# Kernel optimization log

Measured on AMD Instinct MI355X. Metric: run time of the kernel, lower is better.

Reference implementation:

```python
import jax, jax.numpy as jnp
import numpy as np

N_NODES = 100000


def gcn_layer(x, W, b, src, dst, norm, n):
    # x: [N, Fin] -> linear transform then normalized scatter-add aggregation
    h = x @ W                                   # [N, Fout]
    msgs = h[src] * norm[:, None]               # [E+N, Fout] edge messages
    out = jax.ops.segment_sum(msgs, dst, num_segments=n)
    return out + b


def _build_graph(edge_index, n):
    # add self loops (PyG GCNConv default)
    loops = jnp.arange(n, dtype=edge_index.dtype)
    src = jnp.concatenate([edge_index[0], loops])
    dst = jnp.concatenate([edge_index[1], loops])
    deg = jax.ops.segment_sum(jnp.ones_like(dst, dtype=jnp.float32), dst, num_segments=n)
    dis = jnp.where(deg > 0, jax.lax.rsqrt(deg), 0.0)  # deg^{-1/2}
    norm = dis[src] * dis[dst]                  # symmetric normalization per edge
    return src, dst, norm


def setup_inputs() -> dict:
    key = jax.random.key(0)
    ks = jax.random.split(key, 8)
    x = jax.random.normal(ks[0], (N_NODES, 3), dtype=jnp.float32)
    edge_index = jax.random.randint(ks[1], (2, 6400000), 0, N_NODES, dtype=jnp.int32)
    def glorot(k, fin, fout):
        s = jnp.sqrt(6.0 / (fin + fout))
        return jax.random.uniform(k, (fin, fout), jnp.float32, -s, s)
    return {
        "x": x,
        "edge_index": edge_index,
        "W1": glorot(ks[2], 3, 32), "b1": jnp.zeros((32,), jnp.float32),
        "W2": glorot(ks[3], 32, 32), "b2": jnp.zeros((32,), jnp.float32),
        "W3": glorot(ks[4], 32, 1), "b3": jnp.zeros((1,), jnp.float32),
    }


def reference(x, edge_index, W1, b1, W2, b2, W3, b3):
    n = x.shape[0]
    src, dst, norm = _build_graph(edge_index, n)
    h = jax.nn.relu(gcn_layer(x, W1, b1, src, dst, norm, n))
    h = jax.nn.relu(gcn_layer(h, W2, b2, src, dst, norm, n))
    return gcn_layer(h, W3, b3, src, dst, norm, n)
```

## Files before the change

### kernel.cpp

```cpp
#include <hip/hip_runtime.h>
#include <hip/hip_fp16.h>


#define BLK 256
#define SB 1280
#define CHUNK 5000
#define BKT 128
#define NBKT 782
#define MAXNB 1024
#define BUFSZ 15360

__global__ void k_hist(const int* __restrict__ dst, int* __restrict__ hist, int E) {
    __shared__ int lh[NBKT];
    for (int b = threadIdx.x; b < NBKT; b += blockDim.x) lh[b] = 0;
    __syncthreads();
    int beg = blockIdx.x * CHUNK;
    int end = min(E, beg + CHUNK);
    int nq = (end - beg) >> 2;
    const int4* d4 = (const int4*)(dst + beg);
    for (int i = threadIdx.x; i < nq; i += blockDim.x) {
        int4 d = d4[i];
        atomicAdd(&lh[d.x >> 7], 1);
        atomicAdd(&lh[d.y >> 7], 1);
        atomicAdd(&lh[d.z >> 7], 1);
        atomicAdd(&lh[d.w >> 7], 1);
    }
    for (int e = beg + (nq << 2) + threadIdx.x; e < end; e += blockDim.x)
        atomicAdd(&lh[dst[e] >> 7], 1);
    __syncthreads();
    for (int b = threadIdx.x; b < NBKT; b += blockDim.x)
        hist[(size_t)blockIdx.x * NBKT + b] = lh[b];
}

__global__ void k_scanA(int* __restrict__ hist, int* __restrict__ btot, int NB) {
    int b = blockIdx.x, t = threadIdx.x;
    int base = t * 5;
    int v0 = hist[(size_t)(base + 0) * NB + b];
    int v1 = hist[(size_t)(base + 1) * NB + b];
    int v2 = hist[(size_t)(base + 2) * NB + b];
    int v3 = hist[(size_t)(base + 3) * NB + b];
    int v4 = hist[(size_t)(base + 4) * NB + b];
    int s = v0 + v1 + v2 + v3 + v4;
    int lane = t & 63, w = t >> 6;
    int x = s;
#pragma unroll
    for (int off = 1; off < 64; off <<= 1) {
        int u = __shfl_up(x, off, 64);
        if (lane >= off) x += u;
    }
    __shared__ int wsum[4];
    if (lane == 63) wsum[w] = x;
    __syncthreads();
    int woff = 0;
    for (int k = 0; k < 4; k++) woff += (k < w) ? wsum[k] : 0;
    int run = woff + x - s;
    hist[(size_t)(base + 0) * NB + b] = run;  run += v0;
    hist[(size_t)(base + 1) * NB + b] = run;  run += v1;
    hist[(size_t)(base + 2) * NB + b] = run;  run += v2;
    hist[(size_t)(base + 3) * NB + b] = run;  run += v3;
    hist[(size_t)(base + 4) * NB + b] = run;  run += v4;
    if (t == 255) btot[b] = run;
}

__global__ void k_scanB(const int* __restrict__ btot, int* __restrict__ bbase,
                        int NB, int E) {
    __shared__ int sh[MAXNB];
    int t = threadIdx.x;
    int v = (t < NB) ? btot[t] : 0;
    sh[t] = v;
    __syncthreads();
    for (int off = 1; off < MAXNB; off <<= 1) {
        int u = (t >= off) ? sh[t - off] : 0;
        __syncthreads();
        sh[t] += u;
        __syncthreads();
    }
    if (t < NB) bbase[t] = sh[t] - v;
    if (t == 0) bbase[NB] = E;
}

__global__ void k_bsort(const int* __restrict__ src, const int* __restrict__ dst,
                        const int* __restrict__ hist, const int* __restrict__ bbase,
                        unsigned int* __restrict__ packed, int E) {
    __shared__ unsigned int bufB[CHUNK];
    __shared__ unsigned short binarr2[CHUNK];
    __shared__ int cnt[NBKT];
    __shared__ int off[NBKT];
    __shared__ int cur[NBKT];
    __shared__ int gbase[NBKT];
    __shared__ int wsum[4];
    int t = threadIdx.x;
    int beg = blockIdx.x * CHUNK;
    int end = min(E, beg + CHUNK);
    int len = end - beg;
    for (int b = t; b < NBKT; b += blockDim.x) {
        cnt[b] = 0;
        gbase[b] = bbase[b] + hist[(size_t)blockIdx.x * NBKT + b];
    }
    __syncthreads();
    {
        int nq = len >> 2;
        const int4* d4 = (const int4*)(dst + beg);
        for (int i = t; i < nq; i += blockDim.x) {
            int4 d = d4[i];
            atomicAdd(&cnt[d.x >> 7], 1);
            atomicAdd(&cnt[d.y >> 7], 1);
            atomicAdd(&cnt[d.z >> 7], 1);
            atomicAdd(&cnt[d.w >> 7], 1);
        }
        for (int i = (nq << 2) + t; i < len; i += blockDim.x)
            atomicAdd(&cnt[dst[beg + i] >> 7], 1);
    }
    __syncthreads();
    {
        int base = t * 4;
        int v0 = (base + 0 < NBKT) ? cnt[base + 0] : 0;
        int v1 = (base + 1 < NBKT) ? cnt[base + 1] : 0;
        int v2 = (base + 2 < NBKT) ? cnt[base + 2] : 0;
        int v3 = (base + 3 < NBKT) ? cnt[base + 3] : 0;
        int s = v0 + v1 + v2 + v3;
        int lane = t & 63, w = t >> 6;
        int x = s;
#pragma unroll
        for (int o = 1; o < 64; o <<= 1) {
            int u = __shfl_up(x, o, 64);
            if (lane >= o) x += u;
        }
        if (lane == 63) wsum[w] = x;
        __syncthreads();
        int woff = 0;
        for (int k = 0; k < 4; k++) woff += (k < w) ? wsum[k] : 0;
        int run = woff + x - s;
        if (base + 0 < NBKT) { off[base + 0] = run; cur[base + 0] = run; } run += v0;
        if (base + 1 < NBKT) { off[base + 1] = run; cur[base + 1] = run; } run += v1;
        if (base + 2 < NBKT) { off[base + 2] = run; cur[base + 2] = run; } run += v2;
        if (base + 3 < NBKT) { off[base + 3] = run; cur[base + 3] = run; } run += v3;
    }
    __syncthreads();
    for (int i = t; i < len; i += blockDim.x) {
        int d = dst[beg + i];
        int s = src[beg + i];
        int b = d >> 7;
        int pos = atomicAdd(&cur[b], 1);
        bufB[pos] = (unsigned)s | ((unsigned)(d & 127) << 17);
        binarr2[pos] = (unsigned short)b;
    }
    __syncthreads();
    for (int i = t; i < len; i += blockDim.x) {
        int b = binarr2[i];
        packed[gbase[b] + i - off[b]] = bufB[i];
    }
}

__global__ void k_sort(unsigned int* __restrict__ packed, const int* __restrict__ bbase,
                       const float* __restrict__ x, float* __restrict__ dis,
                       float4* __restrict__ y4, int* __restrict__ rowptr, int N, int E) {
    __shared__ unsigned int buf[BUFSZ];
    __shared__ int cnt[4 * BKT];
    __shared__ int cur[4 * BKT];
    __shared__ int wsum[4];
    int b = blockIdx.x, t = threadIdx.x;
    int beg = bbase[b], end = bbase[b + 1];
    int len = end - beg;
    for (int i = t; i < len; i += blockDim.x) buf[i] = packed[beg + i];
    cnt[t] = 0; cnt[t + 256] = 0;
    __syncthreads();
    for (int i = t; i < len; i += blockDim.x) {
        unsigned v = buf[i];
        int key = (int)((v >> 17) << 2) | (int)((v & 0x1FFFFu) >> 15);
        atomicAdd(&cnt[key], 1);
    }
    __syncthreads();
    {
        int v0 = cnt[2 * t], v1 = cnt[2 * t + 1];
        int s = v0 + v1;
        int lane = t & 63, w = t >> 6;
        int xs = s;
#pragma unroll
        for (int o = 1; o < 64; o <<= 1) {
            int u = __shfl_up(xs, o, 64);
            if (lane >= o) xs += u;
        }
        if (lane == 63) wsum[w] = xs;
        __syncthreads();
        int woff = 0;
        for (int k = 0; k < 4; k++) woff += (k < w) ? wsum[k] : 0;
        int run = woff + xs - s;
        cur[2 * t] = run;
        cur[2 * t + 1] = run + v0;
    }
    __syncthreads();
    if (t < BKT) {
        int excl = cur[4 * t];
        int v = cnt[4 * t] + cnt[4 * t + 1] + cnt[4 * t + 2] + cnt[4 * t + 3];
        int gi = b * BKT + t;
        if (gi < N) {
            rowptr[gi] = beg + excl;
            float di = rsqrtf((float)v + 1.0f);
            dis[gi] = di;
            float4 y;
            y.x = di * x[3 * gi + 0];
            y.y = di * x[3 * gi + 1];
            y.z = di * x[3 * gi + 2];
            y.w = 0.0f;
            y4[gi] = y;
        }
    }
    __syncthreads();
    for (int i = t; i < len; i += blockDim.x) {
        unsigned vv = buf[i];
        int key = (int)((vv >> 17) << 2) | (int)((vv & 0x1FFFFu) >> 15);
        int pos = atomicAdd(&cur[key], 1);
        packed[beg + pos] = vv & 0x1FFFF;
    }
    if (b == 0 && t == 0) rowptr[N] = E;
}

__global__ void k_l1(const unsigned int* __restrict__ csr, const int* __restrict__ rowptr,
                     const float4* __restrict__ y4, const float* __restrict__ dis,
                     const float* __restrict__ W1, const float* __restrict__ b1,
                     __half* __restrict__ g, int N) {
    int t = blockIdx.x * blockDim.x + threadIdx.x;
    int i = t >> 5, j = t & 31;
    if (i >= N) return;
    int beg = rowptr[i], end = rowptr[i + 1];
    float ax = 0.f, ay = 0.f, az = 0.f;
    for (int e = beg + j; e < end; e += 32) {
        float4 yv = y4[csr[e]];
        ax += yv.x; ay += yv.y; az += yv.z;
    }
#pragma unroll
    for (int m = 16; m >= 1; m >>= 1) {
        ax += __shfl_xor(ax, m, 32);
        ay += __shfl_xor(ay, m, 32);
        az += __shfl_xor(az, m, 32);
    }
    float di = dis[i];
    float4 ys = y4[i];
    float a0 = di * (ax + ys.x);
    float a1 = di * (ay + ys.y);
    float a2 = di * (az + ys.z);
    float h = b1[j] + a0 * W1[j] + a1 * W1[32 + j] + a2 * W1[64 + j];
    g[(size_t)i * 32 + j] = __float2half(di * fmaxf(h, 0.f));
}

__device__ __forceinline__ void acc4(float& c0, float& c1, float& c2, float& c3,
                                     uint2 r) {
    __half2 a = *(const __half2*)&r.x;
    __half2 b = *(const __half2*)&r.y;
    float2 fa = __half22float2(a);
    float2 fb = __half22float2(b);
    c0 += fa.x; c1 += fa.y; c2 += fb.x; c3 += fb.y;
}

__global__ void k_l2(const unsigned int* __restrict__ csr, const int* __restrict__ rowptr,
                     const __half* __restrict__ g, const float* __restrict__ dis,
                     const float* __restrict__ W2, const float* __restrict__ b2,
                     const float* __restrict__ W3, float* __restrict__ q, int N) {
    int t = blockIdx.x * blockDim.x + threadIdx.x;
    int i = t >> 3, j = t & 7;
    if (i >= N) return;
    int beg = rowptr[i], end = rowptr[i + 1];
    const uint2* g2 = (const uint2*)g;
    float c0 = 0.f, c1 = 0.f, c2 = 0.f, c3 = 0.f;
    int e = beg;
    for (; e + 8 <= end; e += 8) {
        int s0 = (int)csr[e + 0], s1 = (int)csr[e + 1];
        int s2 = (int)csr[e + 2], s3 = (int)csr[e + 3];
        int s4 = (int)csr[e + 4], s5 = (int)csr[e + 5];
        int s6 = (int)csr[e + 6], s7 = (int)csr[e + 7];
        uint2 r0 = g2[s0 * 8 + j];
        uint2 r1 = g2[s1 * 8 + j];
        uint2 r2 = g2[s2 * 8 + j];
        uint2 r3 = g2[s3 * 8 + j];
        uint2 r4 = g2[s4 * 8 + j];
        uint2 r5 = g2[s5 * 8 + j];
        uint2 r6 = g2[s6 * 8 + j];
        uint2 r7 = g2[s7 * 8 + j];
        acc4(c0, c1, c2, c3, r0);
        acc4(c0, c1, c2, c3, r1);
        acc4(c0, c1, c2, c3, r2);
        acc4(c0, c1, c2, c3, r3);
        acc4(c0, c1, c2, c3, r4);
        acc4(c0, c1, c2, c3, r5);
        acc4(c0, c1, c2, c3, r6);
        acc4(c0, c1, c2, c3, r7);
    }
    for (; e < end; e++) {
        int s = (int)csr[e];
        uint2 r = g2[s * 8 + j];
        acc4(c0, c1, c2, c3, r);
    }
    float di = dis[i];
    uint2 rs = g2[i * 8 + j];
    float2 sa = __half22float2(*(const __half2*)&rs.x);
    float2 sb = __half22float2(*(const __half2*)&rs.y);
    float a0 = di * (c0 + sa.x);
    float a1 = di * (c1 + sa.y);
    float a2 = di * (c2 + sb.x);
    float a3 = di * (c3 + sb.y);
    int m = 4 * j;
    float o0 = b2[m + 0], o1 = b2[m + 1], o2 = b2[m + 2], o3 = b2[m + 3];
#pragma unroll
    for (int kl = 0; kl < 8; kl++) {
        float x0 = __shfl(a0, kl, 8);
        float x1 = __shfl(a1, kl, 8);
        float x2 = __shfl(a2, kl, 8);
        float x3 = __shfl(a3, kl, 8);
        const float* w0 = W2 + (4 * kl) * 32 + m;
        o0 = fmaf(x0, w0[0], fmaf(x1, w0[32], fmaf(x2, w0[64], fmaf(x3, w0[96], o0))));
        o1 = fmaf(x0, w0[1], fmaf(x1, w0[33], fmaf(x2, w0[65], fmaf(x3, w0[97], o1))));
        o2 = fmaf(x0, w0[2], fmaf(x1, w0[34], fmaf(x2, w0[66], fmaf(x3, w0[98], o2))));
        o3 = fmaf(x0, w0[3], fmaf(x1, w0[35], fmaf(x2, w0[67], fmaf(x3, w0[99], o3))));
    }
    float cc = fmaxf(o0, 0.f) * W3[m + 0] + fmaxf(o1, 0.f) * W3[m + 1]
             + fmaxf(o2, 0.f) * W3[m + 2] + fmaxf(o3, 0.f) * W3[m + 3];
    cc += __shfl_xor(cc, 1, 8);
    cc += __shfl_xor(cc, 2, 8);
    cc += __shfl_xor(cc, 4, 8);
    if (j == 0) q[i] = di * cc;
}

__global__ void k_l3(const unsigned int* __restrict__ csr, const int* __restrict__ rowptr,
                     const float* __restrict__ q, const float* __restrict__ dis,
                     const float* __restrict__ b3, float* __restrict__ out, int N) {
    int t = blockIdx.x * blockDim.x + threadIdx.x;
    int i = t >> 5, j = t & 31;
    if (i >= N) return;
    int beg = rowptr[i], end = rowptr[i + 1];
    float acc = 0.f;
    for (int e = beg + j; e < end; e += 32)
        acc += q[csr[e]];
#pragma unroll
    for (int m = 16; m >= 1; m >>= 1)
        acc += __shfl_xor(acc, m, 32);
    if (j == 0) out[i] = dis[i] * (acc + q[i]) + b3[0];
}

extern "C" void kernel_launch(void* const* d_in, const int* in_sizes, int n_in,
                              void* d_out, int out_size, void* d_ws, size_t ws_size,
                              hipStream_t stream) {
    const float* x  = (const float*)d_in[0];
    const int*   ei = (const int*)d_in[1];
    const float* W1 = (const float*)d_in[2];
    const float* b1 = (const float*)d_in[3];
    const float* W2 = (const float*)d_in[4];
    const float* b2 = (const float*)d_in[5];
    const float* W3 = (const float*)d_in[6];
    const float* b3 = (const float*)d_in[7];
    float* out = (float*)d_out;

    int N = in_sizes[0] / 3;
    int E = in_sizes[1] / 2;
    const int* src = ei;
    const int* dst = ei + E;

    char* w = (char*)d_ws;
#define CARVE(nbytes) w; w += (((size_t)(nbytes) + 255) & ~(size_t)255)
    int*   hist   = (int*)  CARVE((size_t)SB * NBKT * 4);
    int*   btot   = (int*)  CARVE((size_t)MAXNB * 4);
    int*   bbase  = (int*)  CARVE((size_t)(MAXNB + 1) * 4);
    int*   rowptr = (int*)  CARVE((size_t)(N + 1) * 4);
    float* dis    = (float*)CARVE((size_t)N * 4);
    float* y4     = (float*)CARVE((size_t)N * 16);
    __half* g     = (__half*)CARVE((size_t)N * 32 * 2);
    float* q      = (float*)CARVE((size_t)N * 4);
    unsigned int* packed = (unsigned int*)CARVE((size_t)E * 4);
#undef CARVE

    k_hist <<<SB, BLK, 0, stream>>>(dst, hist, E);
    k_scanA<<<NBKT, BLK, 0, stream>>>(hist, btot, NBKT);
    k_scanB<<<1, MAXNB, 0, stream>>>(btot, bbase, NBKT, E);
    k_bsort<<<SB, BLK, 0, stream>>>(src, dst, hist, bbase, packed, E);
    k_sort <<<NBKT, BLK, 0, stream>>>(packed, bbase, x, dis, (float4*)y4, rowptr, N, E);

    long long tn = (long long)N * 32;
    unsigned gn = (unsigned)((tn + BLK - 1) / BLK);
    long long tn8 = (long long)N * 8;
    unsigned gn8 = (unsigned)((tn8 + BLK - 1) / BLK);
    k_l1<<<gn,  BLK, 0, stream>>>(packed, rowptr, (const float4*)y4, dis, W1, b1, g, N);
    k_l2<<<gn8, BLK, 0, stream>>>(packed, rowptr, g, dis, W2, b2, W3, q, N);
    k_l3<<<gn,  BLK, 0, stream>>>(packed, rowptr, q, dis, b3, out, N);
}
```

Before: 348.8 us.

## Split layer-2 gather into two source-halves passes and reuse histogram counts

Within each destination row, edges are now sorted so sources below 50000 come first, and a per-node midpoint is recorded. Layer-2 aggregation then runs as two kernels: the first gathers only from the lower half of the feature table and writes partial sums, the second gathers from the upper half, adds the partials and applies the dense layers. Each pass touches half of the fp16 feature table, which should improve L2/cache hit rates for the random gathers. The cost is an extra 12.8MB partial write and read, plus a second launch. The bucket-sort kernel also derives per-block bucket counts from adjacent histogram prefix values instead of recounting destinations with shared atomics.

```diff
diff --git a/kernel.cpp b/kernel.cpp
--- a/kernel.cpp
+++ b/kernel.cpp
@@ -9,6 +9,9 @@
 #define NBKT 782
 #define MAXNB 1024
 #define BUFSZ 15360
+#define HALF 50000
+
+typedef float fvec4 __attribute__((ext_vector_type(4)));
 
 __global__ void k_hist(const int* __restrict__ dst, int* __restrict__ hist, int E) {
     __shared__ int lh[NBKT];
@@ -80,7 +83,8 @@
 }
 
 __global__ void k_bsort(const int* __restrict__ src, const int* __restrict__ dst,
-                        const int* __restrict__ hist, const int* __restrict__ bbase,
+                        const int* __restrict__ hist, const int* __restrict__ btot,
+                        const int* __restrict__ bbase,
                         unsigned int* __restrict__ packed, int E) {
     __shared__ unsigned int bufB[CHUNK];
     __shared__ unsigned short binarr2[CHUNK];
@@ -93,23 +97,12 @@
     int beg = blockIdx.x * CHUNK;
     int end = min(E, beg + CHUNK);
     int len = end - beg;
+    int last = (blockIdx.x + 1 == gridDim.x);
     for (int b = t; b < NBKT; b += blockDim.x) {
-        cnt[b] = 0;
-        gbase[b] = bbase[b] + hist[(size_t)blockIdx.x * NBKT + b];
-    }
-    __syncthreads();
-    {
-        int nq = len >> 2;
-        const int4* d4 = (const int4*)(dst + beg);
-        for (int i = t; i < nq; i += blockDim.x) {
-            int4 d = d4[i];
-            atomicAdd(&cnt[d.x >> 7], 1);
-            atomicAdd(&cnt[d.y >> 7], 1);
-            atomicAdd(&cnt[d.z >> 7], 1);
-            atomicAdd(&cnt[d.w >> 7], 1);
-        }
-        for (int i = (nq << 2) + t; i < len; i += blockDim.x)
-            atomicAdd(&cnt[dst[beg + i] >> 7], 1);
+        int my = hist[(size_t)blockIdx.x * NBKT + b];
+        int nx = last ? btot[b] : hist[(size_t)(blockIdx.x + 1) * NBKT + b];
+        cnt[b] = nx - my;
+        gbase[b] = bbase[b] + my;
     }
     __syncthreads();
     {
@@ -154,28 +147,29 @@
 
 __global__ void k_sort(unsigned int* __restrict__ packed, const int* __restrict__ bbase,
                        const float* __restrict__ x, float* __restrict__ dis,
-                       float4* __restrict__ y4, int* __restrict__ rowptr, int N, int E) {
+                       float4* __restrict__ y4, int* __restrict__ rowptr,
+                       int* __restrict__ qmid, int N, int E) {
     __shared__ unsigned int buf[BUFSZ];
-    __shared__ int cnt[4 * BKT];
-    __shared__ int cur[4 * BKT];
+    __shared__ int cnt[2 * BKT];
+    __shared__ int cur[2 * BKT];
     __shared__ int wsum[4];
     int b = blockIdx.x, t = threadIdx.x;
     int beg = bbase[b], end = bbase[b + 1];
     int len = end - beg;
     for (int i = t; i < len; i += blockDim.x) buf[i] = packed[beg + i];
-    cnt[t] = 0; cnt[t + 256] = 0;
+    cnt[t] = 0;
     __syncthreads();
     for (int i = t; i < len; i += blockDim.x) {
         unsigned v = buf[i];
-        int key = (int)((v >> 17) << 2) | (int)((v & 0x1FFFFu) >> 15);
+        int s = (int)(v & 0x1FFFFu);
+        int key = (int)((v >> 17) << 1) | (s >= HALF);
         atomicAdd(&cnt[key], 1);
     }
     __syncthreads();
     {
-        int v0 = cnt[2 * t], v1 = cnt[2 * t + 1];
-        int s = v0 + v1;
+        int v0 = cnt[t];
         int lane = t & 63, w = t >> 6;
-        int xs = s;
+        int xs = v0;
 #pragma unroll
         for (int o = 1; o < 64; o <<= 1) {
             int u = __shfl_up(xs, o, 64);
@@ -185,17 +179,16 @@
         __syncthreads();
         int woff = 0;
         for (int k = 0; k < 4; k++) woff += (k < w) ? wsum[k] : 0;
-        int run = woff + xs - s;
-        cur[2 * t] = run;
-        cur[2 * t + 1] = run + v0;
+        cur[t] = woff + xs - v0;
     }
     __syncthreads();
     if (t < BKT) {
-        int excl = cur[4 * t];
-        int v = cnt[4 * t] + cnt[4 * t + 1] + cnt[4 * t + 2] + cnt[4 * t + 3];
+        int excl = cur[2 * t];
+        int v = cnt[2 * t] + cnt[2 * t + 1];
         int gi = b * BKT + t;
         if (gi < N) {
             rowptr[gi] = beg + excl;
+            qmid[gi]   = beg + cur[2 * t + 1];
             float di = rsqrtf((float)v + 1.0f);
             dis[gi] = di;
             float4 y;
@@ -209,9 +202,10 @@
     __syncthreads();
     for (int i = t; i < len; i += blockDim.x) {
         unsigned vv = buf[i];
-        int key = (int)((vv >> 17) << 2) | (int)((vv & 0x1FFFFu) >> 15);
+        int s = (int)(vv & 0x1FFFFu);
+        int key = (int)((vv >> 17) << 1) | (s >= HALF);
         int pos = atomicAdd(&cur[key], 1);
-        packed[beg + pos] = vv & 0x1FFFF;
+        packed[beg + pos] = (unsigned)s;
     }
     if (b == 0 && t == 0) rowptr[N] = E;
 }
@@ -253,16 +247,10 @@
     c0 += fa.x; c1 += fa.y; c2 += fb.x; c3 += fb.y;
 }
 
-__global__ void k_l2(const unsigned int* __restrict__ csr, const int* __restrict__ rowptr,
-                     const __half* __restrict__ g, const float* __restrict__ dis,
-                     const float* __restrict__ W2, const float* __restrict__ b2,
-                     const float* __restrict__ W3, float* __restrict__ q, int N) {
-    int t = blockIdx.x * blockDim.x + threadIdx.x;
-    int i = t >> 3, j = t & 7;
-    if (i >= N) return;
-    int beg = rowptr[i], end = rowptr[i + 1];
-    const uint2* g2 = (const uint2*)g;
-    float c0 = 0.f, c1 = 0.f, c2 = 0.f, c3 = 0.f;
+__device__ __forceinline__ void gath(const unsigned int* __restrict__ csr,
+                                     const uint2* __restrict__ g2, int j,
+                                     int beg, int end,
+                                     float& c0, float& c1, float& c2, float& c3) {
     int e = beg;
     for (; e + 8 <= end; e += 8) {
         int s0 = (int)csr[e + 0], s1 = (int)csr[e + 1];
@@ -291,6 +279,73 @@
         uint2 r = g2[s * 8 + j];
         acc4(c0, c1, c2, c3, r);
     }
+}
+
+__global__ void k_l2a(const unsigned int* __restrict__ csr, const int* __restrict__ rowptr,
+                      const int* __restrict__ qmid, const __half* __restrict__ g,
+                      fvec4* __restrict__ part4, int N) {
+    int t = blockIdx.x * blockDim.x + threadIdx.x;
+    int i = t >> 3, j = t & 7;
+    if (i >= N) return;
+    float c0 = 0.f, c1 = 0.f, c2 = 0.f, c3 = 0.f;
+    gath(csr, (const uint2*)g, j, rowptr[i], qmid[i], c0, c1, c2, c3);
+    fvec4 p = {c0, c1, c2, c3};
+    __builtin_nontemporal_store(p, &part4[(size_t)i * 8 + j]);
+}
+
+__global__ void k_l2b(const unsigned int* __restrict__ csr, const int* __restrict__ rowptr,
+                      const int* __restrict__ qmid, const __half* __restrict__ g,
+                      const float* __restrict__ dis, const fvec4* __restrict__ part4,
+                      const float* __restrict__ W2, const float* __restrict__ b2,
+                      const float* __restrict__ W3, float* __restrict__ q, int N) {
+    int t = blockIdx.x * blockDim.x + threadIdx.x;
+    int i = t >> 3, j = t & 7;
+    if (i >= N) return;
+    const uint2* g2 = (const uint2*)g;
+    float c0 = 0.f, c1 = 0.f, c2 = 0.f, c3 = 0.f;
+    gath(csr, g2, j, qmid[i], rowptr[i + 1], c0, c1, c2, c3);
+    fvec4 p = __builtin_nontemporal_load(&part4[(size_t)i * 8 + j]);
+    c0 += p.x; c1 += p.y; c2 += p.z; c3 += p.w;
+    float di = dis[i];
+    uint2 rs = g2[i * 8 + j];
+    float2 sa = __half22float2(*(const __half2*)&rs.x);
+    float2 sb = __half22float2(*(const __half2*)&rs.y);
+    float a0 = di * (c0 + sa.x);
+    float a1 = di * (c1 + sa.y);
+    float a2 = di * (c2 + sb.x);
+    float a3 = di * (c3 + sb.y);
+    int m = 4 * j;
+    float o0 = b2[m + 0], o1 = b2[m + 1], o2 = b2[m + 2], o3 = b2[m + 3];
+#pragma unroll
+    for (int kl = 0; kl < 8; kl++) {
+        float x0 = __shfl(a0, kl, 8);
+        float x1 = __shfl(a1, kl, 8);
+        float x2 = __shfl(a2, kl, 8);
+        float x3 = __shfl(a3, kl, 8);
+        const float* w0 = W2 + (4 * kl) * 32 + m;
+        o0 = fmaf(x0, w0[0], fmaf(x1, w0[32], fmaf(x2, w0[64], fmaf(x3, w0[96], o0))));
+        o1 = fmaf(x0, w0[1], fmaf(x1, w0[33], fmaf(x2, w0[65], fmaf(x3, w0[97], o1))));
+        o2 = fmaf(x0, w0[2], fmaf(x1, w0[34], fmaf(x2, w0[66], fmaf(x3, w0[98], o2))));
+        o3 = fmaf(x0, w0[3], fmaf(x1, w0[35], fmaf(x2, w0[67], fmaf(x3, w0[99], o3))));
+    }
+    float cc = fmaxf(o0, 0.f) * W3[m + 0] + fmaxf(o1, 0.f) * W3[m + 1]
+             + fmaxf(o2, 0.f) * W3[m + 2] + fmaxf(o3, 0.f) * W3[m + 3];
+    cc += __shfl_xor(cc, 1, 8);
+    cc += __shfl_xor(cc, 2, 8);
+    cc += __shfl_xor(cc, 4, 8);
+    if (j == 0) q[i] = di * cc;
+}
+
+__global__ void k_l2f(const unsigned int* __restrict__ csr, const int* __restrict__ rowptr,
+                      const __half* __restrict__ g, const float* __restrict__ dis,
+                      const float* __restrict__ W2, const float* __restrict__ b2,
+                      const float* __restrict__ W3, float* __restrict__ q, int N) {
+    int t = blockIdx.x * blockDim.x + threadIdx.x;
+    int i = t >> 3, j = t & 7;
+    if (i >= N) return;
+    const uint2* g2 = (const uint2*)g;
+    float c0 = 0.f, c1 = 0.f, c2 = 0.f, c3 = 0.f;
+    gath(csr, g2, j, rowptr[i], rowptr[i + 1], c0, c1, c2, c3);
     float di = dis[i];
     uint2 rs = g2[i * 8 + j];
     float2 sa = __half22float2(*(const __half2*)&rs.x);
@@ -366,19 +421,31 @@
     __half* g     = (__half*)CARVE((size_t)N * 32 * 2);
     float* q      = (float*)CARVE((size_t)N * 4);
     unsigned int* packed = (unsigned int*)CARVE((size_t)E * 4);
+    int*   qmid   = (int*)  CARVE((size_t)N * 4);
+    fvec4* part4  = (fvec4*)CARVE((size_t)N * 32 * 4);
+    size_t need_split = (size_t)(w - (char*)d_ws);
 #undef CARVE
+    int use_split = (ws_size >= need_split);
+    if (!use_split) qmid = hist;
 
     k_hist <<<SB, BLK, 0, stream>>>(dst, hist, E);
     k_scanA<<<NBKT, BLK, 0, stream>>>(hist, btot, NBKT);
     k_scanB<<<1, MAXNB, 0, stream>>>(btot, bbase, NBKT, E);
-    k_bsort<<<SB, BLK, 0, stream>>>(src, dst, hist, bbase, packed, E);
-    k_sort <<<NBKT, BLK, 0, stream>>>(packed, bbase, x, dis, (float4*)y4, rowptr, N, E);
+    k_bsort<<<SB, BLK, 0, stream>>>(src, dst, hist, btot, bbase, packed, E);
+    k_sort <<<NBKT, BLK, 0, stream>>>(packed, bbase, x, dis, (float4*)y4, rowptr,
+                                      qmid, N, E);
 
     long long tn = (long long)N * 32;
     unsigned gn = (unsigned)((tn + BLK - 1) / BLK);
     long long tn8 = (long long)N * 8;
     unsigned gn8 = (unsigned)((tn8 + BLK - 1) / BLK);
-    k_l1<<<gn,  BLK, 0, stream>>>(packed, rowptr, (const float4*)y4, dis, W1, b1, g, N);
-    k_l2<<<gn8, BLK, 0, stream>>>(packed, rowptr, g, dis, W2, b2, W3, q, N);
-    k_l3<<<gn,  BLK, 0, stream>>>(packed, rowptr, q, dis, b3, out, N);
-}
+    k_l1<<<gn, BLK, 0, stream>>>(packed, rowptr, (const float4*)y4, dis, W1, b1, g, N);
+    if (use_split) {
+        k_l2a<<<gn8, BLK, 0, stream>>>(packed, rowptr, qmid, g, part4, N);
+        k_l2b<<<gn8, BLK, 0, stream>>>(packed, rowptr, qmid, g, dis, part4,
+                                       W2, b2, W3, q, N);
+    } else {
+        k_l2f<<<gn8, BLK, 0, stream>>>(packed, rowptr, g, dis, W2, b2, W3, q, N);
+    }
+    k_l3<<<gn, BLK, 0, stream>>>(packed, rowptr, q, dis, b3, out, N);
+}
```

After: 356.1 us. 2.1% more time.

## Reuse scanned histogram in bucket sort, simplify fine sort, split accumulators

Applied to the files above, without the earlier changes.

k_bsort now derives its per-chunk bucket counts from the exclusive-scanned histogram, taking the next chunk's row or btot for the last block, so it no longer re-reads dst and recounts with shared atomics. k_sort replaces the two-level 512-key sort with a single 128-key counting sort, fuses the global load into the count pass, and shrinks the shared buffer. Both kernels launch with 512 threads. k_l2 spreads its gather accumulation over four independent accumulator sets to shorten the dependent add chains. Risks: the smaller BUFSZ may overflow for heavy buckets, and k_sort now orders each row's edges only by destination rather than also by a coarse source key, which may hurt gather locality in the aggregation layers.

```diff
diff --git a/kernel.cpp b/kernel.cpp
--- a/kernel.cpp
+++ b/kernel.cpp
@@ -3,12 +3,13 @@
 
 
 #define BLK 256
+#define BLK2 512
 #define SB 1280
 #define CHUNK 5000
 #define BKT 128
 #define NBKT 782
 #define MAXNB 1024
-#define BUFSZ 15360
+#define BUFSZ 10240
 
 __global__ void k_hist(const int* __restrict__ dst, int* __restrict__ hist, int E) {
     __shared__ int lh[NBKT];
@@ -80,7 +81,8 @@
 }
 
 __global__ void k_bsort(const int* __restrict__ src, const int* __restrict__ dst,
-                        const int* __restrict__ hist, const int* __restrict__ bbase,
+                        const int* __restrict__ hist, const int* __restrict__ btot,
+                        const int* __restrict__ bbase,
                         unsigned int* __restrict__ packed, int E) {
     __shared__ unsigned int bufB[CHUNK];
     __shared__ unsigned short binarr2[CHUNK];
@@ -88,37 +90,24 @@
     __shared__ int off[NBKT];
     __shared__ int cur[NBKT];
     __shared__ int gbase[NBKT];
-    __shared__ int wsum[4];
+    __shared__ int wsum[8];
     int t = threadIdx.x;
     int beg = blockIdx.x * CHUNK;
     int end = min(E, beg + CHUNK);
     int len = end - beg;
+    int last = (blockIdx.x + 1 == gridDim.x);
     for (int b = t; b < NBKT; b += blockDim.x) {
-        cnt[b] = 0;
-        gbase[b] = bbase[b] + hist[(size_t)blockIdx.x * NBKT + b];
+        int my = hist[(size_t)blockIdx.x * NBKT + b];
+        int nx = last ? btot[b] : hist[(size_t)(blockIdx.x + 1) * NBKT + b];
+        cnt[b] = nx - my;
+        gbase[b] = bbase[b] + my;
     }
     __syncthreads();
     {
-        int nq = len >> 2;
-        const int4* d4 = (const int4*)(dst + beg);
-        for (int i = t; i < nq; i += blockDim.x) {
-            int4 d = d4[i];
-            atomicAdd(&cnt[d.x >> 7], 1);
-            atomicAdd(&cnt[d.y >> 7], 1);
-            atomicAdd(&cnt[d.z >> 7], 1);
-            atomicAdd(&cnt[d.w >> 7], 1);
-        }
-        for (int i = (nq << 2) + t; i < len; i += blockDim.x)
-            atomicAdd(&cnt[dst[beg + i] >> 7], 1);
-    }
-    __syncthreads();
-    {
-        int base = t * 4;
+        int base = t * 2;
         int v0 = (base + 0 < NBKT) ? cnt[base + 0] : 0;
         int v1 = (base + 1 < NBKT) ? cnt[base + 1] : 0;
-        int v2 = (base + 2 < NBKT) ? cnt[base + 2] : 0;
-        int v3 = (base + 3 < NBKT) ? cnt[base + 3] : 0;
-        int s = v0 + v1 + v2 + v3;
+        int s = v0 + v1;
         int lane = t & 63, w = t >> 6;
         int x = s;
 #pragma unroll
@@ -129,12 +118,10 @@
         if (lane == 63) wsum[w] = x;
         __syncthreads();
         int woff = 0;
-        for (int k = 0; k < 4; k++) woff += (k < w) ? wsum[k] : 0;
+        for (int k = 0; k < 8; k++) woff += (k < w) ? wsum[k] : 0;
         int run = woff + x - s;
         if (base + 0 < NBKT) { off[base + 0] = run; cur[base + 0] = run; } run += v0;
         if (base + 1 < NBKT) { off[base + 1] = run; cur[base + 1] = run; } run += v1;
-        if (base + 2 < NBKT) { off[base + 2] = run; cur[base + 2] = run; } run += v2;
-        if (base + 3 < NBKT) { off[base + 3] = run; cur[base + 3] = run; } run += v3;
     }
     __syncthreads();
     for (int i = t; i < len; i += blockDim.x) {
@@ -156,47 +143,40 @@
                        const float* __restrict__ x, float* __restrict__ dis,
                        float4* __restrict__ y4, int* __restrict__ rowptr, int N, int E) {
     __shared__ unsigned int buf[BUFSZ];
-    __shared__ int cnt[4 * BKT];
-    __shared__ int cur[4 * BKT];
-    __shared__ int wsum[4];
+    __shared__ int cnt[BKT];
+    __shared__ int cur[BKT];
+    __shared__ int wsum[2];
     int b = blockIdx.x, t = threadIdx.x;
     int beg = bbase[b], end = bbase[b + 1];
     int len = end - beg;
-    for (int i = t; i < len; i += blockDim.x) buf[i] = packed[beg + i];
-    cnt[t] = 0; cnt[t + 256] = 0;
+    if (t < BKT) cnt[t] = 0;
     __syncthreads();
     for (int i = t; i < len; i += blockDim.x) {
-        unsigned v = buf[i];
-        int key = (int)((v >> 17) << 2) | (int)((v & 0x1FFFFu) >> 15);
-        atomicAdd(&cnt[key], 1);
-    }
-    __syncthreads();
-    {
-        int v0 = cnt[2 * t], v1 = cnt[2 * t + 1];
-        int s = v0 + v1;
-        int lane = t & 63, w = t >> 6;
-        int xs = s;
+        unsigned v = packed[beg + i];
+        buf[i] = v;
+        atomicAdd(&cnt[v >> 17], 1);
+    }
+    __syncthreads();
+    int v0 = 0, xs = 0;
+    if (t < BKT) {
+        v0 = cnt[t];
+        xs = v0;
 #pragma unroll
         for (int o = 1; o < 64; o <<= 1) {
             int u = __shfl_up(xs, o, 64);
-            if (lane >= o) xs += u;
+            if ((t & 63) >= o) xs += u;
         }
-        if (lane == 63) wsum[w] = xs;
-        __syncthreads();
-        int woff = 0;
-        for (int k = 0; k < 4; k++) woff += (k < w) ? wsum[k] : 0;
-        int run = woff + xs - s;
-        cur[2 * t] = run;
-        cur[2 * t + 1] = run + v0;
+        if ((t & 63) == 63) wsum[t >> 6] = xs;
     }
     __syncthreads();
     if (t < BKT) {
-        int excl = cur[4 * t];
-        int v = cnt[4 * t] + cnt[4 * t + 1] + cnt[4 * t + 2] + cnt[4 * t + 3];
+        int woff = (t >= 64) ? wsum[0] : 0;
+        int excl = woff + xs - v0;
+        cur[t] = excl;
         int gi = b * BKT + t;
         if (gi < N) {
             rowptr[gi] = beg + excl;
-            float di = rsqrtf((float)v + 1.0f);
+            float di = rsqrtf((float)v0 + 1.0f);
             dis[gi] = di;
             float4 y;
             y.x = di * x[3 * gi + 0];
@@ -209,8 +189,7 @@
     __syncthreads();
     for (int i = t; i < len; i += blockDim.x) {
         unsigned vv = buf[i];
-        int key = (int)((vv >> 17) << 2) | (int)((vv & 0x1FFFFu) >> 15);
-        int pos = atomicAdd(&cur[key], 1);
+        int pos = atomicAdd(&cur[vv >> 17], 1);
         packed[beg + pos] = vv & 0x1FFFF;
     }
     if (b == 0 && t == 0) rowptr[N] = E;
@@ -262,7 +241,10 @@
     if (i >= N) return;
     int beg = rowptr[i], end = rowptr[i + 1];
     const uint2* g2 = (const uint2*)g;
-    float c0 = 0.f, c1 = 0.f, c2 = 0.f, c3 = 0.f;
+    float pa0 = 0.f, pa1 = 0.f, pa2 = 0.f, pa3 = 0.f;
+    float pb0 = 0.f, pb1 = 0.f, pb2 = 0.f, pb3 = 0.f;
+    float pc0 = 0.f, pc1 = 0.f, pc2 = 0.f, pc3 = 0.f;
+    float pd0 = 0.f, pd1 = 0.f, pd2 = 0.f, pd3 = 0.f;
     int e = beg;
     for (; e + 8 <= end; e += 8) {
         int s0 = (int)csr[e + 0], s1 = (int)csr[e + 1];
@@ -277,20 +259,24 @@
         uint2 r5 = g2[s5 * 8 + j];
         uint2 r6 = g2[s6 * 8 + j];
         uint2 r7 = g2[s7 * 8 + j];
-        acc4(c0, c1, c2, c3, r0);
-        acc4(c0, c1, c2, c3, r1);
-        acc4(c0, c1, c2, c3, r2);
-        acc4(c0, c1, c2, c3, r3);
-        acc4(c0, c1, c2, c3, r4);
-        acc4(c0, c1, c2, c3, r5);
-        acc4(c0, c1, c2, c3, r6);
-        acc4(c0, c1, c2, c3, r7);
+        acc4(pa0, pa1, pa2, pa3, r0);
+        acc4(pb0, pb1, pb2, pb3, r1);
+        acc4(pc0, pc1, pc2, pc3, r2);
+        acc4(pd0, pd1, pd2, pd3, r3);
+        acc4(pa0, pa1, pa2, pa3, r4);
+        acc4(pb0, pb1, pb2, pb3, r5);
+        acc4(pc0, pc1, pc2, pc3, r6);
+        acc4(pd0, pd1, pd2, pd3, r7);
     }
     for (; e < end; e++) {
         int s = (int)csr[e];
         uint2 r = g2[s * 8 + j];
-        acc4(c0, c1, c2, c3, r);
-    }
+        acc4(pa0, pa1, pa2, pa3, r);
+    }
+    float c0 = (pa0 + pb0) + (pc0 + pd0);
+    float c1 = (pa1 + pb1) + (pc1 + pd1);
+    float c2 = (pa2 + pb2) + (pc2 + pd2);
+    float c3 = (pa3 + pb3) + (pc3 + pd3);
     float di = dis[i];
     uint2 rs = g2[i * 8 + j];
     float2 sa = __half22float2(*(const __half2*)&rs.x);
@@ -371,8 +357,8 @@
     k_hist <<<SB, BLK, 0, stream>>>(dst, hist, E);
     k_scanA<<<NBKT, BLK, 0, stream>>>(hist, btot, NBKT);
     k_scanB<<<1, MAXNB, 0, stream>>>(btot, bbase, NBKT, E);
-    k_bsort<<<SB, BLK, 0, stream>>>(src, dst, hist, bbase, packed, E);
-    k_sort <<<NBKT, BLK, 0, stream>>>(packed, bbase, x, dis, (float4*)y4, rowptr, N, E);
+    k_bsort<<<SB, BLK2, 0, stream>>>(src, dst, hist, btot, bbase, packed, E);
+    k_sort <<<NBKT, BLK2, 0, stream>>>(packed, bbase, x, dis, (float4*)y4, rowptr, N, E);
 
     long long tn = (long long)N * 32;
     unsigned gn = (unsigned)((tn + BLK - 1) / BLK);
```

After: 332.2 us. -4.8%, faster.
